# Kernel optimization log

Hardware: AMD Instinct MI355X
Metric: run time of the kernel (lower is better)

## Reference

```python
import math
import jax, jax.numpy as jnp
import numpy as np

B, N, E, H = 1, 4096, 256, 8
D = E // H  # head dim = 32


def setup_inputs() -> dict:
    key = jax.random.key(0)
    ks = jax.random.split(key, 10)
    s = 1.0 / math.sqrt(E)
    return {
        "x": jax.random.normal(ks[0], (B, N, E), dtype=jnp.float32),
        "adjacency": jax.random.randint(ks[1], (B, N, N), 0, 2, dtype=jnp.int32),
        "Wq": jax.random.normal(ks[2], (E, E), dtype=jnp.float32) * s,
        "bq": jnp.zeros((E,), dtype=jnp.float32),
        "Wk": jax.random.normal(ks[3], (E, E), dtype=jnp.float32) * s,
        "bk": jnp.zeros((E,), dtype=jnp.float32),
        "Wv": jax.random.normal(ks[4], (E, E), dtype=jnp.float32) * s,
        "bv": jnp.zeros((E,), dtype=jnp.float32),
        "Wo": jax.random.normal(ks[5], (E, E), dtype=jnp.float32) * s,
        "bo": jnp.zeros((E,), dtype=jnp.float32),
    }


def reference(x, adjacency, Wq, bq, Wk, bk, Wv, bv, Wo, bo):
    b, n, e = x.shape
    # projections (torch Linear: x @ W.T + b), split into heads -> [B,H,N,D]
    def heads(y):
        return y.reshape(b, n, H, D).transpose(0, 2, 1, 3)
    q = heads(x @ Wq.T + bq)
    k = heads(x @ Wk.T + bk)
    v = heads(x @ Wv.T + bv)
    scores = jnp.einsum("bhnd,bhmd->bhnm", q, k) / math.sqrt(D)
    mask = (adjacency[:, None, :, :] == 0)  # [B,1,N,N]
    scores = jnp.where(mask, -jnp.inf, scores)
    w = jax.nn.softmax(scores, axis=-1)
    out = jnp.einsum("bhnm,bhmd->bhnd", w, v)
    out = out.transpose(0, 2, 1, 3).reshape(b, n, e)
    return out @ Wo.T + bo
```

## Files before the change

### kernel.cpp

```cpp
#include <hip/hip_runtime.h>
#include <math.h>


#define NTOK 4096
#define EDIM 256
#define HEADS 8
#define HD 32
#define NSPLIT 2
#define QSCALE 0.17677669529663687f
#define LOG2E 1.4426950408889634f
#define CINIT (-11.541560327111707f)

typedef __attribute__((ext_vector_type(8))) short bf16x8;
typedef __attribute__((ext_vector_type(4))) float f32x4;
typedef __attribute__((ext_vector_type(4))) unsigned long long u64x4;

typedef __attribute__((address_space(3))) unsigned char lds_u8;
typedef const __attribute__((address_space(1))) unsigned char gl_u8;

static __device__ inline short f2bf(float f) {
    unsigned u = __float_as_uint(f);
    u = (u + 0x7FFFu + ((u >> 16) & 1u)) >> 16;
    return (short)u;
}
static __device__ inline unsigned packtrunc(float a, float b) {
    return __builtin_amdgcn_perm(__float_as_uint(b), __float_as_uint(a),
                                 0x07060302u);
}
static __device__ inline float sel_mask(float v, unsigned long long m) {
    float r;
    asm("v_cndmask_b32 %0, 0, %1, %2" : "=v"(r) : "v"(v), "s"(m));
    return r;
}

__global__ __launch_bounds__(256) void prep(
    const int* __restrict__ adj, unsigned long long* __restrict__ maskT,
    const float* __restrict__ x,  const float* __restrict__ Wq,
    const float* __restrict__ Wk, const float* __restrict__ Wv,
    const float* __restrict__ Wo,
    short* __restrict__ xb,  short* __restrict__ wqb,
    short* __restrict__ wkb, short* __restrict__ wvb,
    short* __restrict__ wob)
{
    const int bid = blockIdx.x;
    if (bid < 2048) {
        const int wb = bid * 4 + (threadIdx.x >> 6);
        const int l = threadIdx.x & 63;
        const int lrow = l & 15;
        const int lc4 = ((l >> 4) & 3) * 4;
#pragma unroll
        for (int i = 0; i < 8; ++i) {
            const int w = wb + i * 8192;
            const int qb = w >> 8;
            const int kt = (w >> 2) & 63;
            const int b = w & 3;
            const int row = qb * 16 + lrow;
            const int col = kt * 64 + b * 16 + lc4;
            const int4 av = *(const int4*)&adj[row * NTOK + col];
            const unsigned long long m0 = __ballot(av.x != 0);
            const unsigned long long m1 = __ballot(av.y != 0);
            const unsigned long long m2 = __ballot(av.z != 0);
            const unsigned long long m3 = __ballot(av.w != 0);
            if (l == 0) {
                unsigned long long* dst = &maskT[(size_t)w * 4];
                dst[0] = m0; dst[1] = m1; dst[2] = m2; dst[3] = m3;
            }
        }
    } else {
        const int gid = (bid - 2048) * 256 + threadIdx.x;
        const int e = gid * 4;
        const float* src; short* dst; int off;
        if (e < NTOK * EDIM) { src = x; dst = xb; off = e; }
        else {
            const int r = e - NTOK * EDIM;
            const int wsel = r >> 16;
            off = r & 65535;
            src = (wsel == 0) ? Wq : (wsel == 1) ? Wk : (wsel == 2) ? Wv : Wo;
            dst = (wsel == 0) ? wqb : (wsel == 1) ? wkb : (wsel == 2) ? wvb : wob;
        }
        float4 v = *(const float4*)&src[off];
        uint2 t;
        t.x = (unsigned short)f2bf(v.x) | ((unsigned)(unsigned short)f2bf(v.y) << 16);
        t.y = (unsigned short)f2bf(v.z) | ((unsigned)(unsigned short)f2bf(v.w) << 16);
        *(uint2*)&dst[off] = t;
    }
}

__global__ __launch_bounds__(256) void qkv_mfma(
    const short* __restrict__ xb,
    const short* __restrict__ Wqb, const short* __restrict__ Wkb,
    const short* __restrict__ Wvb,
    const float* __restrict__ bq, const float* __restrict__ bk,
    const float* __restrict__ bv,
    short* __restrict__ qo, short* __restrict__ ko, short* __restrict__ vto)
{
    const int tid = threadIdx.x;
    const int wv = tid >> 6, lane = tid & 63;
    const int grp = lane >> 4, lcol = lane & 15;
    const int wsel = blockIdx.y >> 2;
    const int n0 = (blockIdx.y & 3) << 6;
    const int m0 = blockIdx.x * 64 + wv * 16;
    const short* __restrict__ W = (wsel == 0) ? Wqb : (wsel == 1) ? Wkb : Wvb;
    const float* __restrict__ bias = (wsel == 0) ? bq : (wsel == 1) ? bk : bv;

    bf16x8 af[8];
#pragma unroll
    for (int k = 0; k < 8; ++k)
        af[k] = *(const bf16x8*)&xb[(m0 + lcol) * 256 + k * 32 + grp * 8];

    f32x4 acc[4] = {};
#pragma unroll
    for (int k = 0; k < 8; ++k) {
#pragma unroll
        for (int t = 0; t < 4; ++t) {
            const bf16x8 bt =
                *(const bf16x8*)&W[(n0 + t * 16 + lcol) * 256 + k * 32 + grp * 8];
            acc[t] = __builtin_amdgcn_mfma_f32_16x16x32_bf16(af[k], bt, acc[t], 0, 0, 0);
        }
    }
#pragma unroll
    for (int t = 0; t < 4; ++t) {
        const int feat = n0 + t * 16 + lcol;
        const float bval = bias[feat];
        const int h = feat >> 5, d = feat & 31;
        if (wsel == 2) {
            uint2 o;
            o.x = (unsigned short)f2bf(acc[t][0] + bval) |
                  ((unsigned)(unsigned short)f2bf(acc[t][1] + bval) << 16);
            o.y = (unsigned short)f2bf(acc[t][2] + bval) |
                  ((unsigned)(unsigned short)f2bf(acc[t][3] + bval) << 16);
            *(uint2*)&vto[h * (HD * NTOK) + d * NTOK + m0 + grp * 4] = o;
        } else {
            short* __restrict__ out = (wsel == 0) ? qo : ko;
            const float sc = (wsel == 0) ? (QSCALE * LOG2E) : 1.0f;
#pragma unroll
            for (int j = 0; j < 4; ++j)
                out[h * (NTOK * HD) + (m0 + grp * 4 + j) * HD + d] =
                    f2bf((acc[t][j] + bval) * sc);
        }
    }
}

__global__ __launch_bounds__(256) void attn_mfma(
    const short* __restrict__ qg, const short* __restrict__ kg,
    const short* __restrict__ vtg, const unsigned long long* __restrict__ maskT,
    float* __restrict__ o_part, float* __restrict__ l_part)
{
    const int h = blockIdx.y;
    const int split = blockIdx.z;
    const int q0 = blockIdx.x << 6;
    const short* __restrict__ Q  = qg  + h * (NTOK * HD);
    const short* __restrict__ K  = kg  + h * (NTOK * HD);
    const short* __restrict__ Vt = vtg + h * (HD * NTOK);

    __shared__ short Ks[4][64][32];
    __shared__ short Vs[4][32][64];
    __shared__ short P_lds[2][4][16][76];

    const int tid = threadIdx.x;
    const int wv = tid >> 6;
    const int lane = tid & 63;
    const int grp = lane >> 4;
    const int lcol = lane & 15;
    const int q0w = q0 + wv * 16;
    const int wvu = __builtin_amdgcn_readfirstlane(wv);

    const int k_row = tid >> 2, k_oct = tid & 3;
    const int v_row = tid >> 3;
    const int v_oct = (tid & 7) ^ (v_row & 7);
    const short* __restrict__ kbase = &K[k_row * HD + k_oct * 8];
    const short* __restrict__ vbase = &Vt[v_row * NTOK + v_oct * 8];

    const bf16x8 qfrag = *(const bf16x8*)&Q[(q0w + lcol) * HD + grp * 8];

    const int qb = __builtin_amdgcn_readfirstlane(blockIdx.x * 4 + wv);
    const unsigned long long* __restrict__ mbase = maskT + (size_t)qb * 1024;

    f32x4 ot[2] = {};
    f32x4 lacc = {};
    const f32x4 cinit = {CINIT, CINIT, CINIT, CINIT};
    bf16x8 ones;
#pragma unroll
    for (int i = 0; i < 8; ++i) ones[i] = (short)0x3F80;

    const int tps = 64 / (int)gridDim.z;
    const int kt_begin = split * tps;
    const int kt_end = kt_begin + tps;

#define STAGE(BUF, KT)                                                       \
    {                                                                        \
        const int k0s = (KT) << 6;                                           \
        __builtin_amdgcn_global_load_lds(                                    \
            (gl_u8*)(kbase + k0s * HD),                                      \
            (lds_u8*)((unsigned char*)&Ks[BUF][0][0] + (wvu << 10)),         \
            16, 0, 0);                                                       \
        __builtin_amdgcn_global_load_lds(                                    \
            (gl_u8*)(vbase + k0s),                                           \
            (lds_u8*)((unsigned char*)&Vs[BUF][0][0] + (wvu << 10)),         \
            16, 0, 0);                                                       \
    }

#define TILE(BUF, MP, PP)                                                    \
    {                                                                        \
        const u64x4 wa = (MP)[0], wb = (MP)[1], wc = (MP)[2], wd = (MP)[3];  \
        bf16x8 kf[4], vf[4];                                                 \
        _Pragma("unroll")                                                    \
        for (int b = 0; b < 4; ++b)                                          \
            kf[b] = *(const bf16x8*)&Ks[BUF][b * 16 + lcol][grp * 8];        \
        _Pragma("unroll")                                                    \
        for (int c = 0; c < 2; ++c) {                                        \
            vf[c * 2 + 0] = *(const bf16x8*)                                 \
                &Vs[BUF][c * 16 + lcol][(grp ^ (lcol & 7)) * 8];             \
            vf[c * 2 + 1] = *(const bf16x8*)                                 \
                &Vs[BUF][c * 16 + lcol][((4 + grp) ^ (lcol & 7)) * 8];       \
        }                                                                    \
        f32x4 s[4];                                                          \
        __builtin_amdgcn_s_setprio(1);                                       \
        _Pragma("unroll")                                                    \
        for (int b = 0; b < 4; ++b)                                          \
            s[b] = __builtin_amdgcn_mfma_f32_16x16x32_bf16(                  \
                kf[b], qfrag, cinit, 0, 0, 0);                               \
        __builtin_amdgcn_s_setprio(0);                                       \
        _Pragma("unroll")                                                    \
        for (int b = 0; b < 4; ++b) {                                        \
            const u64x4 wj = (b == 0) ? wa : (b == 1) ? wb                   \
                             : (b == 2) ? wc : wd;                           \
            const float p0 = sel_mask(__builtin_amdgcn_exp2f(s[b][0]), wj[0]); \
            const float p1 = sel_mask(__builtin_amdgcn_exp2f(s[b][1]), wj[1]); \
            const float p2 = sel_mask(__builtin_amdgcn_exp2f(s[b][2]), wj[2]); \
            const float p3 = sel_mask(__builtin_amdgcn_exp2f(s[b][3]), wj[3]); \
            uint2 t;                                                         \
            t.x = packtrunc(p0, p1);                                         \
            t.y = packtrunc(p2, p3);                                         \
            *(uint2*)&P_lds[PP][wv][lcol][b * 16 + grp * 4] = t;             \
        }                                                                    \
        const uint2 pl0 = *(const uint2*)&P_lds[PP][wv][lcol][grp * 8];      \
        const uint2 pl1 = *(const uint2*)&P_lds[PP][wv][lcol][grp * 8 + 4];  \
        const uint2 pl2 = *(const uint2*)&P_lds[PP][wv][lcol][32 + grp * 8]; \
        const uint2 pl3 =                                                    \
            *(const uint2*)&P_lds[PP][wv][lcol][32 + grp * 8 + 4];           \
        struct { uint2 a, b; } u0 = {pl0, pl1}, u1 = {pl2, pl3};             \
        const bf16x8 pf0 = __builtin_bit_cast(bf16x8, u0);                   \
        const bf16x8 pf1 = __builtin_bit_cast(bf16x8, u1);                   \
        __builtin_amdgcn_s_setprio(1);                                       \
        _Pragma("unroll")                                                    \
        for (int c = 0; c < 2; ++c) {                                        \
            ot[c] = __builtin_amdgcn_mfma_f32_16x16x32_bf16(                 \
                vf[c * 2 + 0], pf0, ot[c], 0, 0, 0);                         \
            ot[c] = __builtin_amdgcn_mfma_f32_16x16x32_bf16(                 \
                vf[c * 2 + 1], pf1, ot[c], 0, 0, 0);                         \
        }                                                                    \
        lacc = __builtin_amdgcn_mfma_f32_16x16x32_bf16(ones, pf0, lacc, 0, 0, 0); \
        lacc = __builtin_amdgcn_mfma_f32_16x16x32_bf16(ones, pf1, lacc, 0, 0, 0); \
        __builtin_amdgcn_s_setprio(0);                                       \
    }

    STAGE(0, kt_begin)
    STAGE(1, kt_begin + 1)

    for (int kt = kt_begin; kt < kt_end; kt += 2) {
        asm volatile("s_waitcnt vmcnt(0)" ::: "memory");
        __builtin_amdgcn_s_barrier();
        __builtin_amdgcn_sched_barrier(0);

        const u64x4* mpA = (const u64x4*)(mbase + kt * 16);
        const u64x4* mpB = (const u64x4*)(mbase + kt * 16 + 16);

        if (kt + 2 < kt_end) {
            STAGE((kt + 2) & 3, kt + 2)
            STAGE((kt + 3) & 3, kt + 3)
        }

        TILE(kt & 3, mpA, 0)
        TILE((kt + 1) & 3, mpB, 1)
    }
#undef STAGE
#undef TILE

    float* __restrict__ ob = o_part + split * (NTOK * EDIM);
#pragma unroll
    for (int c = 0; c < 2; ++c) {
        float4 st;
        st.x = ot[c][0]; st.y = ot[c][1]; st.z = ot[c][2]; st.w = ot[c][3];
        *(float4*)&ob[(q0w + lcol) * EDIM + h * HD + c * 16 + grp * 4] = st;
    }
    if (grp == 0)
        l_part[split * (NTOK * HEADS) + (q0w + lcol) * HEADS + h] = lacc[0];
}

template <int NS>
__global__ __launch_bounds__(256) void out_mfma(
    const float* __restrict__ o_part, const float* __restrict__ l_part,
    const short* __restrict__ Wob, const float* __restrict__ bo,
    float* __restrict__ Y)
{
    const int tid = threadIdx.x;
    const int wv = tid >> 6, lane = tid & 63;
    const int grp = lane >> 4, lcol = lane & 15;
    const int n0 = blockIdx.y << 6;
    const int m0 = blockIdx.x * 64 + wv * 16;
    const int r = m0 + lcol;

    bf16x8 af[8];
#pragma unroll
    for (int k = 0; k < 8; ++k) {
        float4 s0 = {0.f, 0.f, 0.f, 0.f}, s1 = {0.f, 0.f, 0.f, 0.f};
        float lv = 0.f;
#pragma unroll
        for (int s = 0; s < NS; ++s) {
            const float* op = &o_part[s * (NTOK * EDIM) + r * EDIM + k * 32 + grp * 8];
            const float4 t0 = *(const float4*)op;
            const float4 t1 = *(const float4*)(op + 4);
            s0.x += t0.x; s0.y += t0.y; s0.z += t0.z; s0.w += t0.w;
            s1.x += t1.x; s1.y += t1.y; s1.z += t1.z; s1.w += t1.w;
            lv += l_part[s * (NTOK * HEADS) + r * HEADS + k];
        }
        const float inv = 1.0f / lv;
        bf16x8 t;
        t[0] = f2bf(s0.x * inv); t[1] = f2bf(s0.y * inv);
        t[2] = f2bf(s0.z * inv); t[3] = f2bf(s0.w * inv);
        t[4] = f2bf(s1.x * inv); t[5] = f2bf(s1.y * inv);
        t[6] = f2bf(s1.z * inv); t[7] = f2bf(s1.w * inv);
        af[k] = t;
    }

    f32x4 acc[4] = {};
#pragma unroll
    for (int k = 0; k < 8; ++k) {
#pragma unroll
        for (int t = 0; t < 4; ++t) {
            const bf16x8 bt =
                *(const bf16x8*)&Wob[(n0 + t * 16 + lcol) * 256 + k * 32 + grp * 8];
            acc[t] = __builtin_amdgcn_mfma_f32_16x16x32_bf16(af[k], bt, acc[t], 0, 0, 0);
        }
    }
#pragma unroll
    for (int t = 0; t < 4; ++t) {
        const float bval = bo[n0 + t * 16 + lcol];
#pragma unroll
        for (int j = 0; j < 4; ++j)
            Y[(m0 + grp * 4 + j) * EDIM + n0 + t * 16 + lcol] = acc[t][j] + bval;
    }
}

extern "C" void kernel_launch(void* const* d_in, const int* in_sizes, int n_in,
                              void* d_out, int out_size, void* d_ws, size_t ws_size,
                              hipStream_t stream) {
    (void)in_sizes; (void)n_in; (void)out_size; (void)ws_size;
    const float* x  = (const float*)d_in[0];
    const int*  adj = (const int*)d_in[1];
    const float* Wq = (const float*)d_in[2];
    const float* bq = (const float*)d_in[3];
    const float* Wk = (const float*)d_in[4];
    const float* bk = (const float*)d_in[5];
    const float* Wv = (const float*)d_in[6];
    const float* bv = (const float*)d_in[7];
    const float* Wo = (const float*)d_in[8];
    const float* bo = (const float*)d_in[9];

    char* ws = (char*)d_ws;
    short* x_bf  = (short*)(ws);
    short* q_ws  = (short*)(ws + (2u << 20));
    short* k_ws  = (short*)(ws + (4u << 20));
    short* vt_ws = (short*)(ws + (6u << 20));
    unsigned long long* maskT =
        (unsigned long long*)(ws + (8u << 20));
    short* Wq_bf = (short*)(ws + (10u << 20));
    short* Wk_bf = Wq_bf + (EDIM * EDIM);
    short* Wv_bf = Wk_bf + (EDIM * EDIM);
    short* Wo_bf = Wv_bf + (EDIM * EDIM);
    float* l_part = (float*)(ws + (11u << 20));
    float* o_part = (float*)(ws + (12u << 20));

    prep<<<dim3(2048 + 1280), 256, 0, stream>>>(
        adj, maskT, x, Wq, Wk, Wv, Wo, x_bf, Wq_bf, Wk_bf, Wv_bf, Wo_bf);
    qkv_mfma<<<dim3(64, 12), 256, 0, stream>>>(x_bf, Wq_bf, Wk_bf, Wv_bf,
                                               bq, bk, bv, q_ws, k_ws, vt_ws);
    attn_mfma<<<dim3(64, HEADS, NSPLIT), 256, 0, stream>>>(
        q_ws, k_ws, vt_ws, maskT, o_part, l_part);
    out_mfma<NSPLIT><<<dim3(64, 4), 256, 0, stream>>>(o_part, l_part, Wo_bf, bo,
                                                      (float*)d_out);
}
```

Measured before the change: 187.4 us.

## Permute V^T token layout to feed P directly from registers, regrid output GEMM

The QKV kernel now writes V^T with tokens permuted inside each 32-token chunk. This lets the attention kernel pass the softmax probabilities from the QK^T MFMA accumulators straight into the PV MFMA as operands, with no LDS round-trip, and the P_lds buffer is removed. The output projection is also regridded: each block now handles 16 rows with its four waves covering all 256 output columns, instead of a 64x4 grid. The intent is to cut LDS traffic and latency in the attention inner loop, which depends on the permutation matching the MFMA operand layout exactly.

Result: faster. 172.8 us (-7.8%).

```diff
diff --git a/kernel.cpp b/kernel.cpp
--- a/kernel.cpp
+++ b/kernel.cpp
@@ -129,7 +129,11 @@
                   ((unsigned)(unsigned short)f2bf(acc[t][1] + bval) << 16);
             o.y = (unsigned short)f2bf(acc[t][2] + bval) |
                   ((unsigned)(unsigned short)f2bf(acc[t][3] + bval) << 16);
-            *(uint2*)&vto[h * (HD * NTOK) + d * NTOK + m0 + grp * 4] = o;
+            const int tb = blockIdx.x * 64;
+            const int tt = (m0 - tb) + grp * 4;
+            const int np = ((tt >> 5) << 5) + ((tt >> 2) & 3) * 8 +
+                           (((tt >> 4) & 1) << 2);
+            *(uint2*)&vto[h * (HD * NTOK) + d * NTOK + tb + np] = o;
         } else {
             short* __restrict__ out = (wsel == 0) ? qo : ko;
             const float sc = (wsel == 0) ? (QSCALE * LOG2E) : 1.0f;
@@ -155,7 +159,6 @@
 
     __shared__ short Ks[4][64][32];
     __shared__ short Vs[4][32][64];
-    __shared__ short P_lds[2][4][16][76];
 
     const int tid = threadIdx.x;
     const int wv = tid >> 6;
@@ -200,7 +203,7 @@
             16, 0, 0);                                                       \
     }
 
-#define TILE(BUF, MP, PP)                                                    \
+#define TILE(BUF, MP)                                                        \
     {                                                                        \
         const u64x4 wa = (MP)[0], wb = (MP)[1], wc = (MP)[2], wd = (MP)[3];  \
         bf16x8 kf[4], vf[4];                                                 \
@@ -221,6 +224,7 @@
             s[b] = __builtin_amdgcn_mfma_f32_16x16x32_bf16(                  \
                 kf[b], qfrag, cinit, 0, 0, 0);                               \
         __builtin_amdgcn_s_setprio(0);                                       \
+        uint2 pk[4];                                                         \
         _Pragma("unroll")                                                    \
         for (int b = 0; b < 4; ++b) {                                        \
             const u64x4 wj = (b == 0) ? wa : (b == 1) ? wb                   \
@@ -229,29 +233,20 @@
             const float p1 = sel_mask(__builtin_amdgcn_exp2f(s[b][1]), wj[1]); \
             const float p2 = sel_mask(__builtin_amdgcn_exp2f(s[b][2]), wj[2]); \
             const float p3 = sel_mask(__builtin_amdgcn_exp2f(s[b][3]), wj[3]); \
-            uint2 t;                                                         \
-            t.x = packtrunc(p0, p1);                                         \
-            t.y = packtrunc(p2, p3);                                         \
-            *(uint2*)&P_lds[PP][wv][lcol][b * 16 + grp * 4] = t;             \
+            pk[b].x = packtrunc(p0, p1);                                     \
+            pk[b].y = packtrunc(p2, p3);                                     \
         }                                                                    \
-        const uint2 pl0 = *(const uint2*)&P_lds[PP][wv][lcol][grp * 8];      \
-        const uint2 pl1 = *(const uint2*)&P_lds[PP][wv][lcol][grp * 8 + 4];  \
-        const uint2 pl2 = *(const uint2*)&P_lds[PP][wv][lcol][32 + grp * 8]; \
-        const uint2 pl3 =                                                    \
-            *(const uint2*)&P_lds[PP][wv][lcol][32 + grp * 8 + 4];           \
-        struct { uint2 a, b; } u0 = {pl0, pl1}, u1 = {pl2, pl3};             \
+        struct U4 { uint2 a, b; };                                           \
+        U4 u0 = {pk[0], pk[1]}, u1 = {pk[2], pk[3]};                         \
         const bf16x8 pf0 = __builtin_bit_cast(bf16x8, u0);                   \
         const bf16x8 pf1 = __builtin_bit_cast(bf16x8, u1);                   \
         __builtin_amdgcn_s_setprio(1);                                       \
-        _Pragma("unroll")                                                    \
-        for (int c = 0; c < 2; ++c) {                                        \
-            ot[c] = __builtin_amdgcn_mfma_f32_16x16x32_bf16(                 \
-                vf[c * 2 + 0], pf0, ot[c], 0, 0, 0);                         \
-            ot[c] = __builtin_amdgcn_mfma_f32_16x16x32_bf16(                 \
-                vf[c * 2 + 1], pf1, ot[c], 0, 0, 0);                         \
-        }                                                                    \
-        lacc = __builtin_amdgcn_mfma_f32_16x16x32_bf16(ones, pf0, lacc, 0, 0, 0); \
-        lacc = __builtin_amdgcn_mfma_f32_16x16x32_bf16(ones, pf1, lacc, 0, 0, 0); \
+        ot[0] = __builtin_amdgcn_mfma_f32_16x16x32_bf16(vf[0], pf0, ot[0], 0, 0, 0); \
+        ot[0] = __builtin_amdgcn_mfma_f32_16x16x32_bf16(vf[1], pf1, ot[0], 0, 0, 0); \
+        ot[1] = __builtin_amdgcn_mfma_f32_16x16x32_bf16(vf[2], pf0, ot[1], 0, 0, 0); \
+        ot[1] = __builtin_amdgcn_mfma_f32_16x16x32_bf16(vf[3], pf1, ot[1], 0, 0, 0); \
+        lacc  = __builtin_amdgcn_mfma_f32_16x16x32_bf16(ones, pf0, lacc, 0, 0, 0);   \
+        lacc  = __builtin_amdgcn_mfma_f32_16x16x32_bf16(ones, pf1, lacc, 0, 0, 0);   \
         __builtin_amdgcn_s_setprio(0);                                       \
     }
 
@@ -271,8 +266,8 @@
             STAGE((kt + 3) & 3, kt + 3)
         }
 
-        TILE(kt & 3, mpA, 0)
-        TILE((kt + 1) & 3, mpB, 1)
+        TILE(kt & 3, mpA)
+        TILE((kt + 1) & 3, mpB)
     }
 #undef STAGE
 #undef TILE
@@ -297,8 +292,8 @@
     const int tid = threadIdx.x;
     const int wv = tid >> 6, lane = tid & 63;
     const int grp = lane >> 4, lcol = lane & 15;
-    const int n0 = blockIdx.y << 6;
-    const int m0 = blockIdx.x * 64 + wv * 16;
+    const int m0 = blockIdx.x << 4;
+    const int n0 = wv << 6;
     const int r = m0 + lcol;
 
     bf16x8 af[8];
@@ -378,6 +373,6 @@
                                                bq, bk, bv, q_ws, k_ws, vt_ws);
     attn_mfma<<<dim3(64, HEADS, NSPLIT), 256, 0, stream>>>(
         q_ws, k_ws, vt_ws, maskT, o_part, l_part);
-    out_mfma<NSPLIT><<<dim3(64, 4), 256, 0, stream>>>(o_part, l_part, Wo_bf, bo,
-                                                      (float*)d_out);
-}
+    out_mfma<NSPLIT><<<dim3(256), 256, 0, stream>>>(o_part, l_part, Wo_bf, bo,
+                                                    (float*)d_out);
+}
```
